# Kernel tuning notes

Hardware: AMD Instinct MI355X
Metric: run time of the kernel (lower is better)

Reference implementation:

```python
import jax, jax.numpy as jnp
import numpy as np

B, H, S, DK = 2, 16, 2048, 64
NEG = jnp.float32(-10000.0)


def setup_inputs() -> dict:
    key = jax.random.key(0)
    kq, kk, kv, km = jax.random.split(key, 4)
    query = jax.random.normal(kq, (B, H, S, DK), dtype=jnp.float32)
    k_ = jax.random.normal(kk, (B, H, S, DK), dtype=jnp.float32)
    value = jax.random.normal(kv, (B, H, S, DK), dtype=jnp.float32)
    mask = (jax.random.uniform(km, (B, 1, S, S)) > 0.5).astype(jnp.float32)
    return {"query": query, "key": k_, "value": value, "mask": mask, "d_k": DK}


def reference(query, key, value, mask, d_k):
    # scores: [B,H,S,S]
    scale = jnp.float32(1.0 / np.sqrt(d_k))
    scores = jnp.einsum('bhqd,bhkd->bhqk', query, key) * scale * mask
    # non-standard masking: keep only strictly positive masked scores
    scores = jnp.where(scores > 0, scores, NEG)
    attn = jax.nn.softmax(scores, axis=-1)
    return jnp.einsum('bhqk,bhkd->bhqd', attn, value)
```

## Files before the change

### kernel.cpp

```cpp
#include <hip/hip_runtime.h>
#include <hip/hip_bf16.h>
#include <math.h>

#define S_LEN 2048
#define D_KV  64
#define BQ    128
#define BK    64
#define LP    72
#define NW    4

typedef __attribute__((ext_vector_type(8)))  short bh8;
typedef __attribute__((ext_vector_type(4)))  short sh4;
typedef __attribute__((ext_vector_type(16))) float f32x16;

__device__ __forceinline__ short f2bf(float f) {
    unsigned u = __builtin_bit_cast(unsigned, f);
    u += 0x7fffu + ((u >> 16) & 1u);
    return (short)(u >> 16);
}

__global__ __launch_bounds__(256, 2)
void attn_fwd(const float* __restrict__ Qg, const float* __restrict__ Kg,
              const float* __restrict__ Vg, const float* __restrict__ Mg,
              float* __restrict__ Og)
{
    __shared__ __align__(16) short k_lds[BK * LP];
    __shared__ __align__(16) short v_lds[D_KV * LP];
    __shared__ __align__(16) short p_lds[NW * 32 * LP];

    const int tid  = threadIdx.x;
    const int wave = tid >> 6;
    const int lane = tid & 63;
    const int n    = lane & 31;
    const int hi   = lane >> 5;

    const int qt = blockIdx.x;
    const int bh = blockIdx.y;
    const int b  = bh >> 4;

    const int qw = qt * BQ + wave * 32;

    const float* Qp = Qg + ((size_t)bh * S_LEN + qw) * D_KV;
    const float* Kp = Kg + (size_t)bh * S_LEN * D_KV;
    const float* Vp = Vg + (size_t)bh * S_LEN * D_KV;
    const float* Mp = Mg + (size_t)b * S_LEN * S_LEN;
    float*       Op = Og + ((size_t)bh * S_LEN + qw) * D_KV;

    bh8 qf[4];
#pragma unroll
    for (int kc = 0; kc < 4; ++kc) {
        const float* src = Qp + n * D_KV + kc * 16 + hi * 8;
        float4 a0 = *(const float4*)(src);
        float4 a1 = *(const float4*)(src + 4);
        bh8 f;
        f[0] = f2bf(a0.x * 0.125f); f[1] = f2bf(a0.y * 0.125f);
        f[2] = f2bf(a0.z * 0.125f); f[3] = f2bf(a0.w * 0.125f);
        f[4] = f2bf(a1.x * 0.125f); f[5] = f2bf(a1.y * 0.125f);
        f[6] = f2bf(a1.z * 0.125f); f[7] = f2bf(a1.w * 0.125f);
        qf[kc] = f;
    }

    f32x16 o0, o1;
    float  l_r[16];
#pragma unroll
    for (int i = 0; i < 16; ++i) { o0[i] = 0.f; o1[i] = 0.f; l_r[i] = 0.f; }

    for (int kt = 0; kt < S_LEN; kt += BK) {
#pragma unroll
        for (int i = 0; i < 4; ++i) {
            int idx = tid + 256 * i;
            int kr  = idx >> 4;
            int db  = (idx & 15) * 4;
            float4 kv = *(const float4*)(Kp + (size_t)(kt + kr) * D_KV + db);
            sh4 s4;
            s4[0] = f2bf(kv.x); s4[1] = f2bf(kv.y);
            s4[2] = f2bf(kv.z); s4[3] = f2bf(kv.w);
            *(sh4*)&k_lds[kr * LP + db] = s4;
        }
        {
            int kr = lane;
#pragma unroll
            for (int i = 0; i < 4; ++i) {
                int db = wave * 16 + i * 4;
                float4 vv = *(const float4*)(Vp + (size_t)(kt + kr) * D_KV + db);
                v_lds[(db + 0) * LP + kr] = f2bf(vv.x);
                v_lds[(db + 1) * LP + kr] = f2bf(vv.y);
                v_lds[(db + 2) * LP + kr] = f2bf(vv.z);
                v_lds[(db + 3) * LP + kr] = f2bf(vv.w);
            }
        }
        __syncthreads();

        f32x16 s0, s1;
#pragma unroll
        for (int i = 0; i < 16; ++i) { s0[i] = 0.f; s1[i] = 0.f; }
#pragma unroll
        for (int kc = 0; kc < 4; ++kc) {
            int off = kc * 16 + hi * 8;
            bh8 b0 = *(const bh8*)&k_lds[n * LP + off];
            bh8 b1 = *(const bh8*)&k_lds[(32 + n) * LP + off];
            s0 = __builtin_amdgcn_mfma_f32_32x32x16_bf16(qf[kc], b0, s0, 0, 0, 0);
            s1 = __builtin_amdgcn_mfma_f32_32x32x16_bf16(qf[kc], b1, s1, 0, 0, 0);
        }

        short* pw = &p_lds[wave * 32 * LP];
        const float* mb = Mp + (size_t)(qw + 4 * hi) * S_LEN + kt + n;
#pragma unroll
        for (int r = 0; r < 16; ++r) {
            int rowo = (r & 3) + 8 * (r >> 2);
            const float* mrow = mb + (size_t)rowo * S_LEN;
            float m0 = mrow[0];
            float m1 = mrow[32];
            float t0 = s0[r] * m0;
            float t1 = s1[r] * m1;
            float p0 = (t0 > 0.f) ? __expf(t0) : 0.f;
            float p1 = (t1 > 0.f) ? __expf(t1) : 0.f;
            l_r[r] += p0 + p1;
            int prow = (rowo + 4 * hi) * LP;
            pw[prow + n]      = f2bf(p0);
            pw[prow + 32 + n] = f2bf(p1);
        }

#pragma unroll
        for (int kc = 0; kc < 4; ++kc) {
            int off = kc * 16 + hi * 8;
            bh8 pa = *(const bh8*)&pw[n * LP + off];
            bh8 v0 = *(const bh8*)&v_lds[n * LP + off];
            bh8 v1 = *(const bh8*)&v_lds[(32 + n) * LP + off];
            o0 = __builtin_amdgcn_mfma_f32_32x32x16_bf16(pa, v0, o0, 0, 0, 0);
            o1 = __builtin_amdgcn_mfma_f32_32x32x16_bf16(pa, v1, o1, 0, 0, 0);
        }
        __syncthreads();
    }

#pragma unroll
    for (int r = 0; r < 16; ++r) {
#pragma unroll
        for (int off = 16; off >= 1; off >>= 1)
            l_r[r] += __shfl_xor(l_r[r], off, 32);
    }

#pragma unroll
    for (int r = 0; r < 16; ++r) {
        int qrow = (r & 3) + 8 * (r >> 2) + 4 * hi;
        float inv = 1.0f / l_r[r];
        Op[(size_t)qrow * D_KV + n]      = o0[r] * inv;
        Op[(size_t)qrow * D_KV + 32 + n] = o1[r] * inv;
    }
}

extern "C" void kernel_launch(void* const* d_in, const int* in_sizes, int n_in,
                              void* d_out, int out_size, void* d_ws, size_t ws_size,
                              hipStream_t stream) {
    const float* Q = (const float*)d_in[0];
    const float* K = (const float*)d_in[1];
    const float* V = (const float*)d_in[2];
    const float* M = (const float*)d_in[3];
    float*       O = (float*)d_out;
    dim3 grid(S_LEN / BQ, 32);
    attn_fwd<<<grid, 256, 0, stream>>>(Q, K, V, M, O);
}
```

Baseline: 229.3 us.

## Split key range across two wave groups per block and reduce partials

```diff
diff --git a/kernel.cpp b/kernel.cpp
--- a/kernel.cpp
+++ b/kernel.cpp
@@ -7,7 +7,7 @@
 #define BQ    128
 #define BK    64
 #define LP    72
-#define NW    4
+#define HALF_S (S_LEN / 2)
 
 typedef __attribute__((ext_vector_type(8)))  short bh8;
 typedef __attribute__((ext_vector_type(4)))  short sh4;
@@ -19,26 +19,34 @@
     return (short)(u >> 16);
 }
 
-__global__ __launch_bounds__(256, 2)
+#define KV_SHORTS (64 * LP)
+#define SMEM_SHORTS (4 * KV_SHORTS + 8 * 32 * LP)
+
+__global__ __launch_bounds__(512, 2)
 void attn_fwd(const float* __restrict__ Qg, const float* __restrict__ Kg,
               const float* __restrict__ Vg, const float* __restrict__ Mg,
               float* __restrict__ Og)
 {
-    __shared__ __align__(16) short k_lds[BK * LP];
-    __shared__ __align__(16) short v_lds[D_KV * LP];
-    __shared__ __align__(16) short p_lds[NW * 32 * LP];
+    __shared__ __align__(16) short smem[SMEM_SHORTS];
 
-    const int tid  = threadIdx.x;
-    const int wave = tid >> 6;
-    const int lane = tid & 63;
-    const int n    = lane & 31;
-    const int hi   = lane >> 5;
+    const int tid   = threadIdx.x;
+    const int wave  = tid >> 6;
+    const int lane  = tid & 63;
+    const int n     = lane & 31;
+    const int hi    = lane >> 5;
+    const int split = wave >> 2;
+    const int qsub  = wave & 3;
+    const int gtid  = tid & 255;
 
     const int qt = blockIdx.x;
     const int bh = blockIdx.y;
     const int b  = bh >> 4;
 
-    const int qw = qt * BQ + wave * 32;
+    const int qw = qt * BQ + qsub * 32;
+
+    short* k_lds = smem + split * 2 * KV_SHORTS;
+    short* v_lds = k_lds + KV_SHORTS;
+    short* pw    = smem + 4 * KV_SHORTS + wave * 32 * LP;
 
     const float* Qp = Qg + ((size_t)bh * S_LEN + qw) * D_KV;
     const float* Kp = Kg + (size_t)bh * S_LEN * D_KV;
@@ -65,10 +73,12 @@
 #pragma unroll
     for (int i = 0; i < 16; ++i) { o0[i] = 0.f; o1[i] = 0.f; l_r[i] = 0.f; }
 
-    for (int kt = 0; kt < S_LEN; kt += BK) {
+    const int kt0 = split * HALF_S;
+    for (int it = 0; it < HALF_S / BK; ++it) {
+        const int kt = kt0 + it * BK;
 #pragma unroll
         for (int i = 0; i < 4; ++i) {
-            int idx = tid + 256 * i;
+            int idx = gtid + 256 * i;
             int kr  = idx >> 4;
             int db  = (idx & 15) * 4;
             float4 kv = *(const float4*)(Kp + (size_t)(kt + kr) * D_KV + db);
@@ -81,7 +91,7 @@
             int kr = lane;
 #pragma unroll
             for (int i = 0; i < 4; ++i) {
-                int db = wave * 16 + i * 4;
+                int db = qsub * 16 + i * 4;
                 float4 vv = *(const float4*)(Vp + (size_t)(kt + kr) * D_KV + db);
                 v_lds[(db + 0) * LP + kr] = f2bf(vv.x);
                 v_lds[(db + 1) * LP + kr] = f2bf(vv.y);
@@ -103,7 +113,6 @@
             s1 = __builtin_amdgcn_mfma_f32_32x32x16_bf16(qf[kc], b1, s1, 0, 0, 0);
         }
 
-        short* pw = &p_lds[wave * 32 * LP];
         const float* mb = Mp + (size_t)(qw + 4 * hi) * S_LEN + kt + n;
 #pragma unroll
         for (int r = 0; r < 16; ++r) {
@@ -133,19 +142,38 @@
         __syncthreads();
     }
 
+    float* fs = (float*)smem;
+    if (split == 1) {
+        float* dst = fs + gtid * 48;
 #pragma unroll
-    for (int r = 0; r < 16; ++r) {
+        for (int i = 0; i < 16; ++i) {
+            dst[i]      = o0[i];
+            dst[16 + i] = o1[i];
+            dst[32 + i] = l_r[i];
+        }
+    }
+    __syncthreads();
+    if (split == 0) {
+        const float* src = fs + gtid * 48;
 #pragma unroll
-        for (int off = 16; off >= 1; off >>= 1)
-            l_r[r] += __shfl_xor(l_r[r], off, 32);
-    }
-
+        for (int i = 0; i < 16; ++i) {
+            o0[i]  += src[i];
+            o1[i]  += src[16 + i];
+            l_r[i] += src[32 + i];
+        }
 #pragma unroll
-    for (int r = 0; r < 16; ++r) {
-        int qrow = (r & 3) + 8 * (r >> 2) + 4 * hi;
-        float inv = 1.0f / l_r[r];
-        Op[(size_t)qrow * D_KV + n]      = o0[r] * inv;
-        Op[(size_t)qrow * D_KV + 32 + n] = o1[r] * inv;
+        for (int r = 0; r < 16; ++r) {
+#pragma unroll
+            for (int off = 16; off >= 1; off >>= 1)
+                l_r[r] += __shfl_xor(l_r[r], off, 32);
+        }
+#pragma unroll
+        for (int r = 0; r < 16; ++r) {
+            int qrow = (r & 3) + 8 * (r >> 2) + 4 * hi;
+            float inv = 1.0f / l_r[r];
+            Op[(size_t)qrow * D_KV + n]      = o0[r] * inv;
+            Op[(size_t)qrow * D_KV + 32 + n] = o1[r] * inv;
+        }
     }
 }
 
@@ -158,5 +186,5 @@
     const float* M = (const float*)d_in[3];
     float*       O = (float*)d_out;
     dim3 grid(S_LEN / BQ, 32);
-    attn_fwd<<<grid, 256, 0, stream>>>(Q, K, V, M, O);
+    attn_fwd<<<grid, 512, 0, stream>>>(Q, K, V, M, O);
 }
```

New measurement: 236.8 us. +3.3%, slower.
